# Kernel optimization log

Measured on AMD Instinct MI355X. Metric: run time of the kernel, lower is better.

## Reference

```python
import jax, jax.numpy as jnp
import numpy as np

D_MODEL = 1024
NUM_HEADS = 16
D_K = D_MODEL // NUM_HEADS
B, S = 2, 2048


def setup_inputs() -> dict:
    key = jax.random.key(0)
    ks = jax.random.split(key, 11)
    scale = 1.0 / np.sqrt(D_MODEL)
    inp = {
        "q": jax.random.normal(ks[0], (B, S, D_MODEL), dtype=jnp.float32),
        "k": jax.random.normal(ks[1], (B, S, D_MODEL), dtype=jnp.float32),
        "v": jax.random.normal(ks[2], (B, S, D_MODEL), dtype=jnp.float32),
        "w_q": jax.random.normal(ks[3], (D_MODEL, D_MODEL), dtype=jnp.float32) * scale,
        "b_q": jnp.zeros((D_MODEL,), dtype=jnp.float32),
        "w_k": jax.random.normal(ks[4], (D_MODEL, D_MODEL), dtype=jnp.float32) * scale,
        "b_k": jnp.zeros((D_MODEL,), dtype=jnp.float32),
        "w_v": jax.random.normal(ks[5], (D_MODEL, D_MODEL), dtype=jnp.float32) * scale,
        "b_v": jnp.zeros((D_MODEL,), dtype=jnp.float32),
        "w_o": jax.random.normal(ks[6], (D_MODEL, D_MODEL), dtype=jnp.float32) * scale,
        "b_o": jnp.zeros((D_MODEL,), dtype=jnp.float32),
    }
    return inp


def reference(q, k, v, w_q, b_q, w_k, b_k, w_v, b_v, w_o, b_o):
    # Linear projections (torch Linear: x @ W^T + b)
    def proj(x, w, b):
        # [B,S,D] -> [B,H,S,d_k]
        y = x @ w.T + b
        return y.reshape(B, S, NUM_HEADS, D_K).transpose(0, 2, 1, 3)

    query = proj(q, w_q, b_q)
    key_ = proj(k, w_k, b_k)
    value = proj(v, w_v, b_v)

    # scores: [B,H,S,S]
    scores = jnp.einsum('bhqd,bhkd->bhqk', query, key_) / jnp.sqrt(
        jnp.asarray(D_K, dtype=query.dtype))
    attn = jax.nn.softmax(scores, axis=-1)
    x = jnp.einsum('bhqk,bhkd->bhqd', attn, value)
    x = x.transpose(0, 2, 1, 3).reshape(B, S, D_MODEL)
    return x @ w_o.T + b_o
```

## Files before the change

### kernel.cpp

```cpp
#include <hip/hip_runtime.h>
#include <stdint.h>

#define D_MODEL 1024
#define NHEAD 16
#define DK 64
#define BATCH 2
#define SEQ 2048
#define MROWS (BATCH * SEQ)
#define KVB 128
#define NIT (SEQ / KVB)
#define QSCALE 0.18033688011112042f

typedef __attribute__((ext_vector_type(8))) __bf16 bf16x8;
typedef __attribute__((ext_vector_type(2))) __bf16 bf16x2;
typedef __attribute__((ext_vector_type(4))) float f32x4;
typedef __attribute__((ext_vector_type(4))) unsigned int u32x4;
typedef __attribute__((ext_vector_type(2))) unsigned int u32x2;

#if defined(__has_builtin)
#if __has_builtin(__builtin_amdgcn_permlane32_swap) && \
    __has_builtin(__builtin_amdgcn_permlane16_swap)
#define HAVE_PERMLANE_SWAP 1
#endif
#endif
#ifndef HAVE_PERMLANE_SWAP
#define HAVE_PERMLANE_SWAP 0
#endif

__device__ __forceinline__ float exp2_hw(float x) {
  return __builtin_amdgcn_exp2f(x);
}

__device__ __forceinline__ f32x4 f4zero() {
  f32x4 z = {0.f, 0.f, 0.f, 0.f};
  return z;
}

__device__ __forceinline__ f32x4 mfma_bf16(bf16x8 a, bf16x8 b, f32x4 c) {
  return __builtin_amdgcn_mfma_f32_16x16x32_bf16(a, b, c, 0, 0, 0);
}

__device__ __forceinline__ void gload_lds16(const void* g, void* l) {
  __builtin_amdgcn_global_load_lds(
      (const __attribute__((address_space(1))) unsigned int*)g,
      (__attribute__((address_space(3))) unsigned int*)l, 16, 0, 0);
}

__device__ __forceinline__ unsigned short f2b(float x) {
  unsigned int u = __float_as_uint(x);
  u += 0x7fffu + ((u >> 16) & 1u);
  return (unsigned short)(u >> 16);
}

#if HAVE_PERMLANE_SWAP
__device__ __forceinline__ u32x2 pl32(unsigned int a, unsigned int b) {
  return __builtin_amdgcn_permlane32_swap(a, b, false, false);
}
__device__ __forceinline__ u32x2 pl16(unsigned int a, unsigned int b) {
  return __builtin_amdgcn_permlane16_swap(a, b, false, false);
}
#endif

__global__ void cvt_w_kernel(const float* __restrict__ wq, const float* __restrict__ wk,
                             const float* __restrict__ wv, const float* __restrict__ wo,
                             unsigned short* __restrict__ wout) {
  const size_t SZW = (size_t)D_MODEL * D_MODEL;
  const int bid = blockIdx.x;
  const int seg = bid >> 10, ib = bid & 1023;
  const float* in = seg == 0 ? wq : seg == 1 ? wk : seg == 2 ? wv : wo;
  unsigned short* out = wout + (size_t)seg * SZW;
  const int i = ib * 256 + threadIdx.x;
  float4 x = ((const float4*)in)[i];
  ushort4 r;
  r.x = f2b(x.x); r.y = f2b(x.y); r.z = f2b(x.z); r.w = f2b(x.w);
  ((ushort4*)out)[i] = r;
}

template <int AF32, int BF32, int BROW>
__device__ __forceinline__ void gemm_body128(const void* __restrict__ Aptr,
                                             const void* __restrict__ Bptr,
                                             const float* __restrict__ bias,
                                             float scale,
                                             unsigned short* __restrict__ outb,
                                             int bm, int bn, int M, int N, int K,
                                             unsigned short* sA, unsigned short* sB) {
  const int tid = threadIdx.x;
  const int w = tid >> 6, l = tid & 63;
  const int rowBase = bm << 7, colBase = bn << 7;
  const int wm = w >> 1, wn = w & 1;
  const int g = l >> 4, c16 = l & 15;

  f32x4 acc[4][4];
#pragma unroll
  for (int i = 0; i < 4; i++)
#pragma unroll
    for (int j = 0; j < 4; j++) acc[i][j] = f4zero();

  const int rloc = l >> 2;
  const int uch = (l & 3) ^ (rloc & 3);
  const int lchunk = l & 3;

  float4 fr[2][2];
  const float* Ff = AF32 ? (const float*)Aptr : (const float*)Bptr;
  const int fBase = AF32 ? rowBase : colBase;

  auto FLOAD = [&](int kk) {
#pragma unroll
    for (int p = 0; p < 2; p++) {
      const size_t base =
          (size_t)(fBase + w * 16 + p * 64 + rloc) * K + kk + uch * 8;
      fr[p][0] = *(const float4*)&Ff[base];
      fr[p][1] = *(const float4*)&Ff[base + 4];
    }
  };
  auto FWRITE = [&](unsigned short* sDst) {
#pragma unroll
    for (int p = 0; p < 2; p++) {
      bf16x8 rr;
      rr[0] = (__bf16)fr[p][0].x; rr[1] = (__bf16)fr[p][0].y;
      rr[2] = (__bf16)fr[p][0].z; rr[3] = (__bf16)fr[p][0].w;
      rr[4] = (__bf16)fr[p][1].x; rr[5] = (__bf16)fr[p][1].y;
      rr[6] = (__bf16)fr[p][1].z; rr[7] = (__bf16)fr[p][1].w;
      *(bf16x8*)&sDst[(w * 16 + p * 64 + rloc) * 32 + lchunk * 8] = rr;
    }
  };

  if (AF32 || BF32) FLOAD(0);

  for (int kk = 0; kk < K; kk += 32) {
    __syncthreads();
    if (AF32) {
      FWRITE(sA);
#pragma unroll
      for (int h = 0; h < 2; h++) {
        const int r0 = w * 16 + h * 64;
        gload_lds16((const unsigned short*)Bptr +
                        (size_t)(colBase + r0 + rloc) * K + kk + uch * 8,
                    &sB[r0 * 32]);
      }
    } else if (BF32) {
#pragma unroll
      for (int h = 0; h < 2; h++) {
        const int r0 = w * 16 + h * 64;
        gload_lds16((const unsigned short*)Aptr +
                        (size_t)(rowBase + r0 + rloc) * K + kk + uch * 8,
                    &sA[r0 * 32]);
      }
      FWRITE(sB);
    } else {
#pragma unroll
      for (int h = 0; h < 2; h++) {
        const int r0 = w * 16 + h * 64;
        gload_lds16((const unsigned short*)Aptr +
                        (size_t)(rowBase + r0 + rloc) * K + kk + uch * 8,
                    &sA[r0 * 32]);
        gload_lds16((const unsigned short*)Bptr +
                        (size_t)(colBase + r0 + rloc) * K + kk + uch * 8,
                    &sB[r0 * 32]);
      }
    }
    __syncthreads();
    if ((AF32 || BF32) && kk + 32 < K) FLOAD(kk + 32);

    bf16x8 af[4], bfr[4];
#pragma unroll
    for (int mt = 0; mt < 4; mt++) {
      const int r = wm * 64 + mt * 16 + c16;
      af[mt] = *(const bf16x8*)&sA[r * 32 + (g ^ (r & 3)) * 8];
    }
#pragma unroll
    for (int nt = 0; nt < 4; nt++) {
      const int r = wn * 64 + nt * 16 + c16;
      bfr[nt] = *(const bf16x8*)&sB[r * 32 + (g ^ (r & 3)) * 8];
    }
#pragma unroll
    for (int mt = 0; mt < 4; mt++)
#pragma unroll
      for (int nt = 0; nt < 4; nt++)
        acc[mt][nt] = mfma_bf16(af[mt], bfr[nt], acc[mt][nt]);
  }

#pragma unroll
  for (int mt = 0; mt < 4; mt++) {
    float brow[4];
    if (BROW) {
#pragma unroll
      for (int i = 0; i < 4; i++)
        brow[i] = bias[rowBase + wm * 64 + mt * 16 + g * 4 + i];
    }
#pragma unroll
    for (int nt = 0; nt < 4; nt++) {
      const int col = colBase + wn * 64 + nt * 16 + c16;
      const float bcol = BROW ? 0.f : bias[col];
#pragma unroll
      for (int i = 0; i < 4; i++) {
        const int row = rowBase + wm * 64 + mt * 16 + g * 4 + i;
        const float bv = BROW ? brow[i] : bcol;
        outb[(size_t)row * N + col] = f2b((acc[mt][nt][i] + bv) * scale);
      }
    }
  }
}

__device__ __forceinline__ void gemm_body64(const unsigned short* __restrict__ A,
                                            const unsigned short* __restrict__ B,
                                            const float* __restrict__ bias,
                                            float* __restrict__ outf, int bx,
                                            int M, int N, int K,
                                            unsigned short* sA, unsigned short* sB) {
  const int tid = threadIdx.x;
  const int w = tid >> 6, l = tid & 63;
  const int nTN = N >> 6;
  const int bm = bx / nTN, bn = bx % nTN;
  const int rowBase = bm << 7, colBase = bn << 6;
  const int g = l >> 4, c16 = l & 15;

  f32x4 acc[2][4];
#pragma unroll
  for (int i = 0; i < 2; i++)
#pragma unroll
    for (int j = 0; j < 4; j++) acc[i][j] = f4zero();

  const int rloc = l >> 2;
  const int uch = (l & 3) ^ (rloc & 3);

  for (int kk = 0; kk < K; kk += 32) {
    __syncthreads();
    gload_lds16(A + (size_t)(rowBase + w * 16 + rloc) * K + kk + uch * 8,
                &sA[(w * 16) * 32]);
    gload_lds16(A + (size_t)(rowBase + 64 + w * 16 + rloc) * K + kk + uch * 8,
                &sA[(64 + w * 16) * 32]);
    gload_lds16(B + (size_t)(colBase + w * 16 + rloc) * K + kk + uch * 8,
                &sB[(w * 16) * 32]);
    __syncthreads();

    bf16x8 af[2], bfr[4];
#pragma unroll
    for (int mt = 0; mt < 2; mt++) {
      const int r = w * 32 + mt * 16 + c16;
      af[mt] = *(const bf16x8*)&sA[r * 32 + (g ^ (r & 3)) * 8];
    }
#pragma unroll
    for (int nt = 0; nt < 4; nt++) {
      const int r = nt * 16 + c16;
      bfr[nt] = *(const bf16x8*)&sB[r * 32 + (g ^ (r & 3)) * 8];
    }
#pragma unroll
    for (int mt = 0; mt < 2; mt++)
#pragma unroll
      for (int nt = 0; nt < 4; nt++)
        acc[mt][nt] = mfma_bf16(af[mt], bfr[nt], acc[mt][nt]);
  }

#pragma unroll
  for (int mt = 0; mt < 2; mt++)
#pragma unroll
    for (int nt = 0; nt < 4; nt++) {
      const int col = colBase + nt * 16 + c16;
      const float bv = bias[col];
#pragma unroll
      for (int i = 0; i < 4; i++) {
        const int row = rowBase + w * 32 + mt * 16 + g * 4 + i;
        outf[(size_t)row * N + col] = acc[mt][nt][i] + bv;
      }
    }
}

__global__ __launch_bounds__(256, 3) void gemm_qkv_kernel(
    const float* __restrict__ qin, const float* __restrict__ kin,
    const float* __restrict__ vin, const unsigned short* __restrict__ Wbase,
    const float* __restrict__ bq, const float* __restrict__ bk,
    const float* __restrict__ bv, unsigned short* __restrict__ QKout,
    unsigned short* __restrict__ VTout) {
  __shared__ __attribute__((aligned(16))) unsigned short sA[128 * 32];
  __shared__ __attribute__((aligned(16))) unsigned short sB[128 * 32];
  const int gid = blockIdx.x >> 8, rb = blockIdx.x & 255;
  const int c = rb & 7, j = rb >> 3;
  const size_t SZA = (size_t)MROWS * D_MODEL;
  const size_t SZW = (size_t)D_MODEL * D_MODEL;
  if (gid < 2) {
    const int bm = c * 4 + (j >> 3), bn = j & 7;
    const float* act = gid == 0 ? qin : kin;
    const float* bias = gid == 0 ? bq : bk;
    const float scale = gid == 0 ? QSCALE : 1.0f;
    gemm_body128<1, 0, 0>(act, Wbase + (size_t)gid * SZW, bias, scale,
                          QKout + (size_t)gid * SZA, bm, bn, MROWS, D_MODEL,
                          D_MODEL, sA, sB);
  } else {
    const int bm = j & 7, bn = c * 4 + (j >> 3);
    gemm_body128<0, 1, 1>(Wbase + 2 * SZW, vin, bv, 1.0f, VTout, bm, bn,
                          D_MODEL, MROWS, D_MODEL, sA, sB);
  }
}

__global__ __launch_bounds__(256, 4) void gemm_out_kernel(
    const unsigned short* __restrict__ A, const unsigned short* __restrict__ B,
    const float* __restrict__ bias, float* __restrict__ out) {
  __shared__ __attribute__((aligned(16))) unsigned short sA[128 * 32];
  __shared__ __attribute__((aligned(16))) unsigned short sB[64 * 32];
  gemm_body64(A, B, bias, out, blockIdx.x, MROWS, D_MODEL, D_MODEL, sA, sB);
}

__global__ __launch_bounds__(256, 2) void attn_kernel(
    const unsigned short* __restrict__ Qh, const unsigned short* __restrict__ Kh,
    const unsigned short* __restrict__ Vt, unsigned short* __restrict__ Xh) {
  __shared__ __attribute__((aligned(16))) unsigned short sK[2][2][64 * 64];
  __shared__ __attribute__((aligned(16))) unsigned short sV[2][2][64 * 64];

  const int tid = threadIdx.x, w = tid >> 6, l = tid & 63;
  const int fid = blockIdx.x;
  const int L = (fid & 7) * 64 + (fid >> 3);
  const int bh = L >> 4, qx = L & 15;
  const int b = bh >> 4, h = bh & 15;
  const int q0 = qx * 128 + w * 32;
  const int g = l >> 4, c16 = l & 15;

  bf16x8 qf[2][2];
#pragma unroll
  for (int qs = 0; qs < 2; ++qs)
#pragma unroll
    for (int f = 0; f < 2; ++f)
      qf[qs][f] = *(const bf16x8*)&Qh[(size_t)(b * SEQ + q0 + qs * 16 + c16) * D_MODEL +
                                      h * DK + f * 32 + g * 8];

  const u32x4 onesu = {0x3F803F80u, 0x3F803F80u, 0x3F803F80u, 0x3F803F80u};
  const bf16x8 onesf = __builtin_bit_cast(bf16x8, onesu);

  f32x4 acc[2][4], accl[2];
#pragma unroll
  for (int qs = 0; qs < 2; ++qs) {
#pragma unroll
    for (int dt = 0; dt < 4; ++dt) acc[qs][dt] = f4zero();
    accl[qs] = f4zero();
  }

  const int srow = l >> 3, sch = (l & 7) ^ (srow & 7);

  auto STAGE = [&](int pbuf, int kv0) {
#pragma unroll
    for (int half = 0; half < 2; ++half)
#pragma unroll
      for (int hh = 0; hh < 2; ++hh) {
        const int r0 = w * 16 + hh * 8;
        const int kvh = kv0 + half * 64;
        gload_lds16(
            Kh + (size_t)(b * SEQ + kvh + r0 + srow) * D_MODEL + h * DK + sch * 8,
            &sK[pbuf][half][r0 * 64]);
        gload_lds16(
            Vt + (size_t)(h * DK + r0 + srow) * MROWS + b * SEQ + kvh + sch * 8,
            &sV[pbuf][half][r0 * 64]);
      }
  };

  auto STEPH = [&](const unsigned short* sKp, const unsigned short* sVp) {
    f32x4 st[2][4];
#pragma unroll
    for (int kt = 0; kt < 4; ++kt) {
      bf16x8 kf[2];
#pragma unroll
      for (int f = 0; f < 2; ++f) {
        const int key = kt * 16 + c16;
        const int ch = (f * 4 + g) ^ (key & 7);
        kf[f] = *(const bf16x8*)&sKp[key * 64 + ch * 8];
      }
#pragma unroll
      for (int qs = 0; qs < 2; ++qs) {
        f32x4 s = mfma_bf16(kf[0], qf[qs][0], f4zero());
        st[qs][kt] = mfma_bf16(kf[1], qf[qs][1], s);
      }
    }

    unsigned int Qpk[2][4][2];
#pragma unroll
    for (int qs = 0; qs < 2; ++qs)
#pragma unroll
      for (int kt = 0; kt < 4; ++kt) {
        float pv[4];
#pragma unroll
        for (int i = 0; i < 4; ++i) pv[i] = exp2_hw(st[qs][kt][i]);
#pragma unroll
        for (int hh = 0; hh < 2; ++hh) {
          bf16x2 t2;
          t2.x = (__bf16)pv[hh * 2];
          t2.y = (__bf16)pv[hh * 2 + 1];
          Qpk[qs][kt][hh] = __builtin_bit_cast(unsigned int, t2);
        }
      }

#pragma unroll
    for (int ks = 0; ks < 2; ++ks) {
      bf16x8 pfrag[2];
#pragma unroll
      for (int qs = 0; qs < 2; ++qs) {
        unsigned int pw[4];
#if HAVE_PERMLANE_SWAP
#pragma unroll
        for (int hh = 0; hh < 2; ++hh) {
          u32x2 s1 = pl32(Qpk[qs][2 * ks][hh], Qpk[qs][2 * ks + 1][hh]);
          u32x2 s2 = pl16(s1.x, s1.y);
          pw[hh] = s2.x;
          pw[2 + hh] = s2.y;
        }
#else
#pragma unroll
        for (int hh = 0; hh < 2; ++hh) {
          const unsigned int a = Qpk[qs][2 * ks][hh], bb = Qpk[qs][2 * ks + 1][hh];
          const unsigned int as = __shfl_xor((int)a, 32);
          const unsigned int bs = __shfl_xor((int)bb, 32);
          const unsigned int r0 = (l >= 32) ? bs : a;
          const unsigned int r1 = (l >= 32) ? bb : as;
          const unsigned int t0 = __shfl_xor((int)r0, 16);
          const unsigned int t1 = __shfl_xor((int)r1, 16);
          pw[hh] = (g & 1) ? t1 : r0;
          pw[2 + hh] = (g & 1) ? r1 : t0;
        }
#endif
        u32x4 pv4 = {pw[0], pw[1], pw[2], pw[3]};
        pfrag[qs] = __builtin_bit_cast(bf16x8, pv4);
      }
      __builtin_amdgcn_s_setprio(1);
      accl[0] = mfma_bf16(pfrag[0], onesf, accl[0]);
      accl[1] = mfma_bf16(pfrag[1], onesf, accl[1]);
#pragma unroll
      for (int dt = 0; dt < 4; ++dt) {
        const int d = dt * 16 + c16;
        const int ch = (ks * 4 + g) ^ (d & 7);
        bf16x8 vfrag = *(const bf16x8*)&sVp[d * 64 + ch * 8];
        acc[0][dt] = mfma_bf16(pfrag[0], vfrag, acc[0][dt]);
        acc[1][dt] = mfma_bf16(pfrag[1], vfrag, acc[1][dt]);
      }
      __builtin_amdgcn_s_setprio(0);
    }
  };

  STAGE(0, 0);
  __syncthreads();

  for (int it = 0; it < NIT; it += 2) {
    if (it + 1 < NIT) STAGE(1, (it + 1) * KVB);
    STEPH(&sK[0][0][0], &sV[0][0][0]);
    STEPH(&sK[0][1][0], &sV[0][1][0]);
    __syncthreads();
    if (it + 2 < NIT) STAGE(0, (it + 2) * KVB);
    STEPH(&sK[1][0][0], &sV[1][0][0]);
    STEPH(&sK[1][1][0], &sV[1][1][0]);
    __syncthreads();
  }

#pragma unroll
  for (int qs = 0; qs < 2; ++qs) {
    float linv[4];
#pragma unroll
    for (int i = 0; i < 4; ++i) linv[i] = __builtin_amdgcn_rcpf(accl[qs][i]);
#pragma unroll
    for (int dt = 0; dt < 4; ++dt)
#pragma unroll
      for (int i = 0; i < 4; ++i) {
        const int row = b * SEQ + q0 + qs * 16 + g * 4 + i;
        const int col = h * DK + dt * 16 + c16;
        Xh[(size_t)row * D_MODEL + col] = f2b(acc[qs][dt][i] * linv[i]);
      }
  }
}

extern "C" void kernel_launch(void* const* d_in, const int* in_sizes, int n_in,
                              void* d_out, int out_size, void* d_ws, size_t ws_size,
                              hipStream_t stream) {
  (void)in_sizes; (void)n_in; (void)out_size; (void)ws_size;
  const float* q = (const float*)d_in[0];
  const float* k = (const float*)d_in[1];
  const float* v = (const float*)d_in[2];
  const float* w_q = (const float*)d_in[3];
  const float* b_q = (const float*)d_in[4];
  const float* w_k = (const float*)d_in[5];
  const float* b_k = (const float*)d_in[6];
  const float* w_v = (const float*)d_in[7];
  const float* b_v = (const float*)d_in[8];
  const float* w_o = (const float*)d_in[9];
  const float* b_o = (const float*)d_in[10];

  const size_t SZ_ACT = (size_t)MROWS * D_MODEL;
  const size_t SZ_W = (size_t)D_MODEL * D_MODEL;
  char* ws = (char*)d_ws;
  unsigned short* Xh = (unsigned short*)(ws);
  unsigned short* Qproj = (unsigned short*)(ws + 6 * SZ_ACT);
  unsigned short* Vt = (unsigned short*)(ws + 10 * SZ_ACT);
  unsigned short* wqb = (unsigned short*)(ws + 12 * SZ_ACT);
  unsigned short* wob = (unsigned short*)(ws + 12 * SZ_ACT + 6 * SZ_W);

  cvt_w_kernel<<<4096, 256, 0, stream>>>(w_q, w_k, w_v, w_o, wqb);

  gemm_qkv_kernel<<<3 * 256, 256, 0, stream>>>(q, k, v, wqb, b_q, b_k, b_v,
                                               Qproj, Vt);

  attn_kernel<<<512, 256, 0, stream>>>(Qproj, Qproj + SZ_ACT, Vt, Xh);

  gemm_out_kernel<<<512, 256, 0, stream>>>(Xh, wob, b_o, (float*)d_out);
}
```

Baseline: 110.0 us.

## Double-buffer LDS tiles in QKV projection GEMM to overlap loads with MFMA

Replaces the single-buffered k-loop in the 128x128 GEMM body with two LDS buffers: the next k-tile's global-to-LDS loads and fp32 register prefetch are issued before computing on the current tile, and each step needs only one barrier instead of two. This hides global load latency behind MFMA work. LDS use per block doubles (32 KB), and launch bounds are raised from 3 to 4 blocks per CU, which increases register pressure.

```diff
diff --git a/kernel.cpp b/kernel.cpp
--- a/kernel.cpp
+++ b/kernel.cpp
@@ -83,12 +83,16 @@
                                              float scale,
                                              unsigned short* __restrict__ outb,
                                              int bm, int bn, int M, int N, int K,
-                                             unsigned short* sA, unsigned short* sB) {
+                                             unsigned short* sA0, unsigned short* sA1,
+                                             unsigned short* sB0, unsigned short* sB1) {
   const int tid = threadIdx.x;
   const int w = tid >> 6, l = tid & 63;
   const int rowBase = bm << 7, colBase = bn << 7;
   const int wm = w >> 1, wn = w & 1;
   const int g = l >> 4, c16 = l & 15;
+
+  unsigned short* sAb[2] = {sA0, sA1};
+  unsigned short* sBb[2] = {sB0, sB1};
 
   f32x4 acc[4][4];
 #pragma unroll
@@ -124,60 +128,62 @@
       *(bf16x8*)&sDst[(w * 16 + p * 64 + rloc) * 32 + lchunk * 8] = rr;
     }
   };
-
-  if (AF32 || BF32) FLOAD(0);
-
-  for (int kk = 0; kk < K; kk += 32) {
-    __syncthreads();
-    if (AF32) {
-      FWRITE(sA);
-#pragma unroll
-      for (int h = 0; h < 2; h++) {
-        const int r0 = w * 16 + h * 64;
+  auto GLOADS = [&](int kk, unsigned short* sDstA, unsigned short* sDstB) {
+#pragma unroll
+    for (int h = 0; h < 2; h++) {
+      const int r0 = w * 16 + h * 64;
+      if (!AF32)
+        gload_lds16((const unsigned short*)Aptr +
+                        (size_t)(rowBase + r0 + rloc) * K + kk + uch * 8,
+                    &sDstA[r0 * 32]);
+      if (!BF32)
         gload_lds16((const unsigned short*)Bptr +
                         (size_t)(colBase + r0 + rloc) * K + kk + uch * 8,
-                    &sB[r0 * 32]);
-      }
-    } else if (BF32) {
-#pragma unroll
-      for (int h = 0; h < 2; h++) {
-        const int r0 = w * 16 + h * 64;
-        gload_lds16((const unsigned short*)Aptr +
-                        (size_t)(rowBase + r0 + rloc) * K + kk + uch * 8,
-                    &sA[r0 * 32]);
-      }
-      FWRITE(sB);
-    } else {
-#pragma unroll
-      for (int h = 0; h < 2; h++) {
-        const int r0 = w * 16 + h * 64;
-        gload_lds16((const unsigned short*)Aptr +
-                        (size_t)(rowBase + r0 + rloc) * K + kk + uch * 8,
-                    &sA[r0 * 32]);
-        gload_lds16((const unsigned short*)Bptr +
-                        (size_t)(colBase + r0 + rloc) * K + kk + uch * 8,
-                    &sB[r0 * 32]);
-      }
-    }
-    __syncthreads();
-    if ((AF32 || BF32) && kk + 32 < K) FLOAD(kk + 32);
-
+                    &sDstB[r0 * 32]);
+    }
+  };
+  auto COMPUTE = [&](const unsigned short* sAr, const unsigned short* sBr) {
     bf16x8 af[4], bfr[4];
 #pragma unroll
     for (int mt = 0; mt < 4; mt++) {
       const int r = wm * 64 + mt * 16 + c16;
-      af[mt] = *(const bf16x8*)&sA[r * 32 + (g ^ (r & 3)) * 8];
+      af[mt] = *(const bf16x8*)&sAr[r * 32 + (g ^ (r & 3)) * 8];
     }
 #pragma unroll
     for (int nt = 0; nt < 4; nt++) {
       const int r = wn * 64 + nt * 16 + c16;
-      bfr[nt] = *(const bf16x8*)&sB[r * 32 + (g ^ (r & 3)) * 8];
+      bfr[nt] = *(const bf16x8*)&sBr[r * 32 + (g ^ (r & 3)) * 8];
     }
 #pragma unroll
     for (int mt = 0; mt < 4; mt++)
 #pragma unroll
       for (int nt = 0; nt < 4; nt++)
         acc[mt][nt] = mfma_bf16(af[mt], bfr[nt], acc[mt][nt]);
+  };
+
+  if (AF32 || BF32) FLOAD(0);
+  GLOADS(0, sAb[0], sBb[0]);
+  if (AF32) FWRITE(sAb[0]);
+  else if (BF32) FWRITE(sBb[0]);
+  __syncthreads();
+
+  auto STEP = [&](int kk, int cur) {
+    const int nxt = cur ^ 1;
+    const bool more = kk + 32 < K;
+    if (more) {
+      if (AF32 || BF32) FLOAD(kk + 32);
+      GLOADS(kk + 32, sAb[nxt], sBb[nxt]);
+    }
+    COMPUTE(sAb[cur], sBb[cur]);
+    if (more) {
+      if (AF32) FWRITE(sAb[nxt]);
+      else if (BF32) FWRITE(sBb[nxt]);
+    }
+    __syncthreads();
+  };
+  for (int kk = 0; kk < K; kk += 64) {
+    STEP(kk, 0);
+    STEP(kk + 32, 1);
   }
 
 #pragma unroll
@@ -266,14 +272,14 @@
     }
 }
 
-__global__ __launch_bounds__(256, 3) void gemm_qkv_kernel(
+__global__ __launch_bounds__(256, 4) void gemm_qkv_kernel(
     const float* __restrict__ qin, const float* __restrict__ kin,
     const float* __restrict__ vin, const unsigned short* __restrict__ Wbase,
     const float* __restrict__ bq, const float* __restrict__ bk,
     const float* __restrict__ bv, unsigned short* __restrict__ QKout,
     unsigned short* __restrict__ VTout) {
-  __shared__ __attribute__((aligned(16))) unsigned short sA[128 * 32];
-  __shared__ __attribute__((aligned(16))) unsigned short sB[128 * 32];
+  __shared__ __attribute__((aligned(16))) unsigned short sA[2][128 * 32];
+  __shared__ __attribute__((aligned(16))) unsigned short sB[2][128 * 32];
   const int gid = blockIdx.x >> 8, rb = blockIdx.x & 255;
   const int c = rb & 7, j = rb >> 3;
   const size_t SZA = (size_t)MROWS * D_MODEL;
@@ -285,11 +291,11 @@
     const float scale = gid == 0 ? QSCALE : 1.0f;
     gemm_body128<1, 0, 0>(act, Wbase + (size_t)gid * SZW, bias, scale,
                           QKout + (size_t)gid * SZA, bm, bn, MROWS, D_MODEL,
-                          D_MODEL, sA, sB);
+                          D_MODEL, sA[0], sA[1], sB[0], sB[1]);
   } else {
     const int bm = j & 7, bn = c * 4 + (j >> 3);
     gemm_body128<0, 1, 1>(Wbase + 2 * SZW, vin, bv, 1.0f, VTout, bm, bn,
-                          D_MODEL, MROWS, D_MODEL, sA, sB);
+                          D_MODEL, MROWS, D_MODEL, sA[0], sA[1], sB[0], sB[1]);
   }
 }
 
```

After: 112.6 us. +2.4%, slower.
